# Kernel optimization log

Measured on AMD Instinct MI355X. Metric: run time of the kernel, lower is better.

## Reference

```python
import jax, jax.numpy as jnp
import numpy as np
import math

B = 2
D_MODEL = 2048
L_MAX = 4096
FILTER_ORDER = 64
EMB_DIM = 3
SHORT_K = 3


def setup_inputs() -> dict:
    key = jax.random.key(0)
    ks = jax.random.split(key, 16)
    D = D_MODEL

    def n(k, shape, scale=0.02):
        return jax.random.normal(k, shape, dtype=jnp.float32) * scale

    return {
        "x": jax.random.normal(ks[0], (B, L_MAX, D), dtype=jnp.float32),
        "in_proj_w": n(ks[1], (3 * D, D)),
        "in_proj_b": n(ks[2], (3 * D,)),
        "short_w": n(ks[3], (3 * D, 1, SHORT_K), 0.3),   # depthwise conv weight (O, I/groups=1, K)
        "short_b": n(ks[4], (3 * D,), 0.1),
        "mlp_w0": n(ks[5], (FILTER_ORDER, EMB_DIM), 0.5),
        "mlp_b0": n(ks[6], (FILTER_ORDER,), 0.5),
        "sin_freq": jnp.ones((1, FILTER_ORDER), dtype=jnp.float32),  # Sin module, w=1, shared across MLP layers
        "mlp_w1": n(ks[7], (FILTER_ORDER, FILTER_ORDER), 0.1),
        "mlp_b1": n(ks[8], (FILTER_ORDER,), 0.1),
        "mlp_w2": n(ks[9], (FILTER_ORDER, FILTER_ORDER), 0.1),
        "mlp_b2": n(ks[10], (FILTER_ORDER,), 0.1),
        "mlp_w3": n(ks[11], (D, FILTER_ORDER), 0.1),      # final Linear(order -> d_model, bias=False)
        "filter_bias": jax.random.normal(ks[12], (D,), dtype=jnp.float32),  # HyenaFilter.bias ~ randn
        "out_proj_w": n(ks[13], (D, D)),
        "out_proj_b": n(ks[14], (D,)),
    }


def _pos_emb(L):
    # PositionalEmbedding: t in [0,1], 1 complex band (emb_dim=3 -> bands=1)
    t = jnp.linspace(0.0, 1.0, L)[:, None]               # (L, 1)
    t_resc = jnp.linspace(0.0, L - 1.0, L)
    w = 2.0 * math.pi * t_resc / L                       # (L,)
    bands = (EMB_DIM - 1) // 2
    f = jnp.linspace(1e-4, bands - 1.0, bands)           # (bands,)
    ang = f[None, :] * w[:, None]                        # (L, bands)
    # z = exp(-1j * f * w) -> real = cos, imag = -sin
    z = jnp.concatenate([t, jnp.cos(ang), -jnp.sin(ang)], axis=-1)  # (L, 3)
    return z, t


def _filter_k(L, w0, b0, freq, w1, b1, w2, b2, w3):
    z, t = _pos_emb(L)
    h = jnp.sin(freq * (z @ w0.T + b0))
    h = jnp.sin(freq * (h @ w1.T + b1))
    h = jnp.sin(freq * (h @ w2.T + b2))
    h = h @ w3.T                                         # (L, D)
    # ExponentialModulation: deltas = linspace(log(.01)/1.5, log(.01)/0.3, D)
    max_decay = math.log(0.01) / 0.3
    min_decay = math.log(0.01) / 1.5
    deltas = jnp.linspace(min_decay, max_decay, h.shape[-1])
    decay = jnp.exp(-t * jnp.abs(deltas)[None, :])       # (L, D)
    return (h * decay).T                                 # (D, L)


def _fftconv(u, k, bias):
    # fftconv_ref with gelu=False, no dropout_mask: u (B, D, L), k (D, L), bias (D,)
    L = u.shape[-1]
    n = 2 * L
    k_f = jnp.fft.rfft(k, n=n) / n                       # (D, L+1)
    u_f = jnp.fft.rfft(u, n=n)                           # (B, D, L+1)
    y = jnp.fft.irfft(u_f * k_f, n=n, norm="forward")[..., :L]
    return y + u * bias[:, None]


def reference(x, in_proj_w, in_proj_b, short_w, short_b, mlp_w0, mlp_b0, sin_freq,
              mlp_w1, mlp_b1, mlp_w2, mlp_b2, mlp_w3, filter_bias,
              out_proj_w, out_proj_b):
    Bn, L, D = x.shape
    u = x @ in_proj_w.T + in_proj_b                      # (B, L, 3D)
    u = jnp.transpose(u, (0, 2, 1))                      # (B, 3D, L)
    # depthwise short conv, padding = short_k - 1, truncate to L (causal-ish)
    uc = jax.lax.conv_general_dilated(
        u, short_w, window_strides=(1,),
        padding=[(SHORT_K - 1, SHORT_K - 1)],
        feature_group_count=3 * D,
        dimension_numbers=("NCH", "OIH", "NCH"))
    uc = uc[..., :L] + short_b[None, :, None]
    x0, x1, v = jnp.split(uc, 3, axis=1)                 # each (B, D, L)
    k = _filter_k(L, mlp_w0, mlp_b0, sin_freq, mlp_w1, mlp_b1, mlp_w2, mlp_b2, mlp_w3)
    # order=2 Hyena recurrence: single gated long-conv step
    v = v * x1
    v = _fftconv(v, k, filter_bias)
    y = v * x0                                           # (B, D, L)
    y = jnp.transpose(y, (0, 2, 1))                      # (B, L, D)
    return y @ out_proj_w.T + out_proj_b
```

## Files before the change

### kernel.cpp

```cpp
#include <hip/hip_runtime.h>
#include <hip/hip_bf16.h>
#include <cstdint>
#include <cstddef>

typedef __attribute__((ext_vector_type(8))) short    bf16x8;
typedef __attribute__((ext_vector_type(4))) float    f32x4;
typedef __attribute__((ext_vector_type(8))) unsigned short u16x8;
typedef __attribute__((ext_vector_type(4))) float    f32v4;
typedef __attribute__((ext_vector_type(4))) unsigned short u16v4;

__device__ __forceinline__ float b2f(unsigned short v) {
    return __builtin_bit_cast(float, ((unsigned int)v) << 16);
}
__device__ __forceinline__ unsigned short f2b(float f) {
    unsigned int u = __builtin_bit_cast(unsigned int, f);
    u += 0x7fffu + ((u >> 16) & 1u);
    return (unsigned short)(u >> 16);
}

__device__ __forceinline__ void async16(const void* g, void* l) {
    __builtin_amdgcn_global_load_lds(
        (const __attribute__((address_space(1))) unsigned int*)g,
        (__attribute__((address_space(3))) unsigned int*)l, 16, 0, 0);
}

__global__ __launch_bounds__(256) void cvt_f32_bf16(const float* __restrict__ src,
                                                    unsigned short* __restrict__ dst, int n4) {
    int i = blockIdx.x * blockDim.x + threadIdx.x;
    int stride = gridDim.x * blockDim.x;
    const f32v4* s4 = (const f32v4*)src;
    u16v4* d4 = (u16v4*)dst;
    for (; i < n4; i += stride) {
        f32v4 v = s4[i];
        u16v4 o;
        o.x = f2b(v.x); o.y = f2b(v.y); o.z = f2b(v.z); o.w = f2b(v.w);
        d4[i] = o;
    }
}

template <int MODE>
__global__ __launch_bounds__(512, 1) void gemm256(
    const unsigned short* __restrict__ A,
    const unsigned short* __restrict__ Bw,
    const float* __restrict__ bias,
    void* __restrict__ Cout,
    int M, int N, int K, int Lseq, int CH, int ntn)
{
    constexpr int SMEM_BYTES = (MODE == 1) ? 135168 : 131072;
    __shared__ char smemc[SMEM_BYTES];

    const int tid = threadIdx.x;
    const int w   = tid >> 6;
    const int l   = tid & 63;
    const int wm  = w & 1;
    const int wn  = w >> 1;
    const int quad = l >> 4;
    const int lq   = l & 15;

    int id = blockIdx.x;
    const int q8 = gridDim.x >> 3;
    id = (id & 7) * q8 + (id >> 3);
    const int bx = id % ntn, by = id / ntn;
    const int n0 = bx * 256, m0 = by * 256;

    const int su0 = quad ^ (lq & 7);
    const int su1 = su0 ^ 4;

    uint32_t offAe[2][2], offBe[2][2];
    int dA[2][2], dB[2][2];
    #pragma unroll
    for (int h = 0; h < 2; ++h)
        #pragma unroll
        for (int c = 0; c < 2; ++c) {
            const int Lr = h * 128 + w * 16 + c * 8 + (l >> 3);
            const int gA = ((Lr & 64) << 1) | ((Lr & 128) >> 1) | (Lr & 63);
            const int u  = (l & 7) ^ (l >> 3);
            offAe[h][c] = (uint32_t)(m0 + gA) * (uint32_t)K + (uint32_t)(u * 8);
            offBe[h][c] = (uint32_t)(n0 + Lr) * (uint32_t)K + (uint32_t)(u * 8);
            const int rb = (h * 128 + w * 16 + c * 8) * 128;
            dA[h][c] = rb;
            dB[h][c] = 32768 + rb;
        }

#define STAGE_A(bs, h, tile) do { \
    async16(A + offAe[h][0] + (size_t)(tile) * 64, smemc + ((bs) * 65536 + dA[h][0])); \
    async16(A + offAe[h][1] + (size_t)(tile) * 64, smemc + ((bs) * 65536 + dA[h][1])); \
} while (0)
#define STAGE_B(bs, h, tile) do { \
    async16(Bw + offBe[h][0] + (size_t)(tile) * 64, smemc + ((bs) * 65536 + dB[h][0])); \
    async16(Bw + offBe[h][1] + (size_t)(tile) * 64, smemc + ((bs) * 65536 + dB[h][1])); \
} while (0)

    f32x4 acc[8][4] = {};
    bf16x8 bw[4][2], a[2][2];

#define LDB8(bs) do { \
    _Pragma("unroll") for (int j = 0; j < 4; ++j) { \
        const int Lr = wn * 64 + j * 16 + lq; \
        bw[j][0] = *(const bf16x8*)(smemc + (bs) * 65536 + 32768 + Lr * 128 + su0 * 16); \
        bw[j][1] = *(const bf16x8*)(smemc + (bs) * 65536 + 32768 + Lr * 128 + su1 * 16); \
    } } while (0)
#define LDA4(bs, q) do { \
    _Pragma("unroll") for (int mf = 0; mf < 2; ++mf) { \
        const int g = wm * 128 + (q) * 32 + mf * 16 + lq; \
        const int Lr = ((g & 64) << 1) | ((g & 128) >> 1) | (g & 63); \
        a[mf][0] = *(const bf16x8*)(smemc + (bs) * 65536 + Lr * 128 + su0 * 16); \
        a[mf][1] = *(const bf16x8*)(smemc + (bs) * 65536 + Lr * 128 + su1 * 16); \
    } } while (0)
#define MFMA16(q) do { \
    _Pragma("unroll") for (int mf = 0; mf < 2; ++mf) \
    _Pragma("unroll") for (int j = 0; j < 4; ++j) \
    _Pragma("unroll") for (int kk = 0; kk < 2; ++kk) \
        acc[(q) * 2 + mf][j] = __builtin_amdgcn_mfma_f32_16x16x32_bf16(a[mf][kk], bw[j][kk], acc[(q) * 2 + mf][j], 0, 0, 0); \
} while (0)
#define PHASE_SYNC() do { \
    __builtin_amdgcn_s_barrier(); \
    asm volatile("s_waitcnt lgkmcnt(0)" ::: "memory"); \
    __builtin_amdgcn_sched_barrier(0); \
    __builtin_amdgcn_s_setprio(1); \
} while (0)
#define PHASE_END() do { \
    __builtin_amdgcn_s_setprio(0); \
    __builtin_amdgcn_s_barrier(); \
} while (0)
#define PHASE_END_DRAIN(lastf) do { \
    __builtin_amdgcn_s_setprio(0); \
    if (lastf) asm volatile("s_waitcnt vmcnt(0)" ::: "memory"); \
    else       asm volatile("s_waitcnt vmcnt(6)" ::: "memory"); \
    __builtin_amdgcn_s_barrier(); \
} while (0)

    STAGE_B(0, 0, 0); STAGE_B(0, 1, 0); STAGE_A(0, 0, 0); STAGE_A(0, 1, 0);
    STAGE_B(1, 0, 1); STAGE_B(1, 1, 1); STAGE_A(1, 0, 1);
    asm volatile("s_waitcnt vmcnt(6)" ::: "memory");
    __builtin_amdgcn_s_barrier();

    const int nIt = K >> 7;
    for (int i = 0; i < nIt; ++i) {
        const bool last = (i == nIt - 1);
        const int t0 = 2 * i, t1 = 2 * i + 1;
        LDB8(0); LDA4(0, 0); STAGE_A(1, 1, t1);
        PHASE_SYNC(); MFMA16(0); PHASE_END();
        LDA4(0, 1); if (!last) STAGE_B(0, 0, t0 + 2);
        PHASE_SYNC(); MFMA16(1); PHASE_END();
        LDA4(0, 2); if (!last) STAGE_B(0, 1, t0 + 2);
        PHASE_SYNC(); MFMA16(2); PHASE_END();
        LDA4(0, 3); if (!last) STAGE_A(0, 0, t0 + 2);
        PHASE_SYNC(); MFMA16(3); PHASE_END_DRAIN(last);
        LDB8(1); LDA4(1, 0); if (!last) STAGE_A(0, 1, t0 + 2);
        PHASE_SYNC(); MFMA16(0); PHASE_END();
        LDA4(1, 1); if (!last) STAGE_B(1, 0, t1 + 2);
        PHASE_SYNC(); MFMA16(1); PHASE_END();
        LDA4(1, 2); if (!last) STAGE_B(1, 1, t1 + 2);
        PHASE_SYNC(); MFMA16(2); PHASE_END();
        LDA4(1, 3); if (!last) STAGE_A(1, 0, t1 + 2);
        PHASE_SYNC(); MFMA16(3); PHASE_END_DRAIN(last);
    }

    if (MODE == 0) {
        float* out = (float*)Cout;
        #pragma unroll
        for (int j = 0; j < 4; ++j) {
            const int col = n0 + wn * 64 + j * 16 + lq;
            const float bv = bias[col];
            #pragma unroll
            for (int i8 = 0; i8 < 8; ++i8) {
                const int rowb = m0 + wm * 128 + i8 * 16 + quad * 4;
                f32x4 c = acc[i8][j];
                out[(size_t)(rowb + 0) * N + col] = c.x + bv;
                out[(size_t)(rowb + 1) * N + col] = c.y + bv;
                out[(size_t)(rowb + 2) * N + col] = c.z + bv;
                out[(size_t)(rowb + 3) * N + col] = c.w + bv;
            }
        }
    } else {
        unsigned short* sE = (unsigned short*)smemc;
        __syncthreads();
        #pragma unroll
        for (int j = 0; j < 4; ++j) {
            const int nl = wn * 64 + j * 16 + lq;
            const float bv = bias[n0 + nl];
            #pragma unroll
            for (int i8 = 0; i8 < 8; ++i8) {
                const int ml = wm * 128 + i8 * 16 + quad * 4;
                f32x4 c = acc[i8][j];
                u16v4 pk;
                pk.x = f2b(c.x + bv); pk.y = f2b(c.y + bv);
                pk.z = f2b(c.z + bv); pk.w = f2b(c.w + bv);
                *(u16v4*)&sE[nl * 264 + ml] = pk;
            }
        }
        __syncthreads();
        unsigned short* uo = (unsigned short*)Cout;
        const int bI = m0 >> 12;
        const int l0 = m0 & 4095;
        for (int e = tid; e < 8192; e += 512) {
            const int nl = e >> 5, seg = e & 31;
            u16x8 v = *(const u16x8*)&sE[nl * 264 + seg * 8];
            *(u16x8*)&uo[(size_t)(bI * CH + n0 + nl) * Lseq + l0 + seg * 8] = v;
        }
    }
#undef STAGE_A
#undef STAGE_B
#undef LDB8
#undef LDA4
#undef MFMA16
#undef PHASE_SYNC
#undef PHASE_END
#undef PHASE_END_DRAIN
}

__global__ __launch_bounds__(256) void filter_kernel(
    const float* __restrict__ w0, const float* __restrict__ b0,
    const float* __restrict__ freq,
    const float* __restrict__ w1, const float* __restrict__ b1,
    const float* __restrict__ w2, const float* __restrict__ b2,
    const float* __restrict__ w3, float* __restrict__ kf)
{
    __shared__ float ha[64][64];
    __shared__ float hb[64][64];
    const int tid = threadIdx.x;
    const int l0 = blockIdx.x * 64;
    const int d0 = blockIdx.y * 256;
    const int l  = tid & 63;
    const int lg = l0 + l;
    const float tt = (float)lg * (1.0f / 4095.0f);
    const float wang = 6.283185307179586f * (float)lg * (1.0f / 4096.0f);
    const float a  = 1e-4f * wang;
    const float z0 = tt, z1 = cosf(a), z2 = -sinf(a);

    for (int e = tid; e < 4096; e += 256) {
        const int dim = e >> 6;
        float pre = z0 * w0[dim * 3] + z1 * w0[dim * 3 + 1] + z2 * w0[dim * 3 + 2] + b0[dim];
        ha[dim][l] = sinf(freq[dim] * pre);
    }
    __syncthreads();
    for (int e = tid; e < 4096; e += 256) {
        const int dim = e >> 6;
        float acc = b1[dim];
        #pragma unroll
        for (int jj = 0; jj < 64; ++jj) acc += w1[dim * 64 + jj] * ha[jj][l];
        hb[dim][l] = sinf(freq[dim] * acc);
    }
    __syncthreads();
    for (int e = tid; e < 4096; e += 256) {
        const int dim = e >> 6;
        float acc = b2[dim];
        #pragma unroll
        for (int jj = 0; jj < 64; ++jj) acc += w2[dim * 64 + jj] * hb[jj][l];
        ha[dim][l] = sinf(freq[dim] * acc);
    }
    __syncthreads();
    for (int d = d0 + (tid >> 6); d < d0 + 256; d += 4) {
        float acc = 0.f;
        #pragma unroll
        for (int jj = 0; jj < 64; ++jj) acc += w3[d * 64 + jj] * ha[jj][l];
        const float delta = fabsf(-3.0701134573253944f + (-5.999245642062483e-3f) * (float)d);
        kf[(size_t)d * 4096 + lg] = acc * __expf(-tt * delta);
    }
}

#define PIDX(i) ((i) + ((i) >> 5))

__device__ __forceinline__ void bfly_f(float& r1, float& i1, float& r2, float& i2, float wr, float wi) {
    float ur = r1, ui = i1, vr = r2, vi = i2;
    r1 = ur + vr; i1 = ui + vi;
    float dr = ur - vr, di = ui - vi;
    r2 = dr * wr - di * wi;
    i2 = dr * wi + di * wr;
}
__device__ __forceinline__ void bfly_i(float& r1, float& i1, float& r2, float& i2, float wr, float wi) {
    float vr = r2 * wr - i2 * wi, vi = r2 * wi + i2 * wr;
    float ur = r1, ui = i1;
    r1 = ur + vr; i1 = ui + vi;
    r2 = ur - vr; i2 = ui - vi;
}

template <int DS, int STR>
__device__ __forceinline__ void fwd_stage(float* re, float* im, int tt) {
    float wr[8], wi[8];
    constexpr float c = -3.14159265358979f / (float)(STR * DS);
    #pragma unroll
    for (int k = 0; k < DS; ++k) __sincosf(c * (float)(tt + STR * k), &wi[k], &wr[k]);
    #pragma unroll
    for (int s = 0; s < 16; ++s)
        if ((s & DS) == 0)
            bfly_f(re[s], im[s], re[s + DS], im[s + DS], wr[s & (DS - 1)], wi[s & (DS - 1)]);
}
template <int DS, int STR>
__device__ __forceinline__ void inv_stage(float* re, float* im, int tt) {
    float wr[8], wi[8];
    constexpr float c = 3.14159265358979f / (float)(STR * DS);
    #pragma unroll
    for (int k = 0; k < DS; ++k) __sincosf(c * (float)(tt + STR * k), &wi[k], &wr[k]);
    #pragma unroll
    for (int s = 0; s < 16; ++s)
        if ((s & DS) == 0)
            bfly_i(re[s], im[s], re[s + DS], im[s + DS], wr[s & (DS - 1)], wi[s & (DS - 1)]);
}

__device__ __forceinline__ void xchg(float* re, float* im, float* fre, float* fim,
                                     int wbase, int wstr, int rbase, int rstr) {
    __syncthreads();
    #pragma unroll
    for (int s = 0; s < 16; ++s) {
        const int i = wbase + wstr * s;
        fre[PIDX(i)] = re[s]; fim[PIDX(i)] = im[s];
    }
    __syncthreads();
    #pragma unroll
    for (int s = 0; s < 16; ++s) {
        const int i = rbase + rstr * s;
        re[s] = fre[PIDX(i)]; im[s] = fim[PIDX(i)];
    }
}

__device__ __forceinline__ void fwd_fft(float* re, float* im, float* fre, float* fim, int t) {
    const int off = t & 31, seg = t >> 5;
    fwd_stage<8, 512>(re, im, t);
    fwd_stage<4, 512>(re, im, t);
    fwd_stage<2, 512>(re, im, t);
    fwd_stage<1, 512>(re, im, t);
    xchg(re, im, fre, fim, t, 512, seg * 512 + off, 32);
    fwd_stage<8, 32>(re, im, off);
    fwd_stage<4, 32>(re, im, off);
    fwd_stage<2, 32>(re, im, off);
    fwd_stage<1, 32>(re, im, off);
    {
        float wr, wi;
        __sincosf(-3.14159265358979f * (float)(off & 15) / 16.0f, &wi, &wr);
        const bool hi = (off & 16) != 0;
        #pragma unroll
        for (int s = 0; s < 16; ++s) {
            float rr = __shfl_xor(re[s], 16);
            float ri = __shfl_xor(im[s], 16);
            if (!hi) { re[s] += rr; im[s] += ri; }
            else {
                float dr = rr - re[s], di = ri - im[s];
                re[s] = dr * wr - di * wi;
                im[s] = dr * wi + di * wr;
            }
        }
    }
    xchg(re, im, fre, fim, seg * 512 + off, 32, 16 * t, 1);
    fwd_stage<8, 1>(re, im, 0);
    fwd_stage<4, 1>(re, im, 0);
    fwd_stage<2, 1>(re, im, 0);
    fwd_stage<1, 1>(re, im, 0);
}

__device__ __forceinline__ void inv_fft(float* re, float* im, float* fre, float* fim, int t) {
    const int off = t & 31, seg = t >> 5;
    inv_stage<1, 1>(re, im, 0);
    inv_stage<2, 1>(re, im, 0);
    inv_stage<4, 1>(re, im, 0);
    inv_stage<8, 1>(re, im, 0);
    xchg(re, im, fre, fim, 16 * t, 1, seg * 512 + off, 32);
    {
        float wr, wi;
        __sincosf(3.14159265358979f * (float)(off & 15) / 16.0f, &wi, &wr);
        const bool hi = (off & 16) != 0;
        #pragma unroll
        for (int s = 0; s < 16; ++s) {
            float rr = __shfl_xor(re[s], 16);
            float ri = __shfl_xor(im[s], 16);
            if (!hi) {
                float vr = rr * wr - ri * wi, vi = rr * wi + ri * wr;
                re[s] += vr; im[s] += vi;
            } else {
                float vr = re[s] * wr - im[s] * wi, vi = re[s] * wi + im[s] * wr;
                re[s] = rr - vr; im[s] = ri - vi;
            }
        }
    }
    inv_stage<1, 32>(re, im, off);
    inv_stage<2, 32>(re, im, off);
    inv_stage<4, 32>(re, im, off);
    inv_stage<8, 32>(re, im, off);
    xchg(re, im, fre, fim, seg * 512 + off, 32, t, 512);
    inv_stage<1, 512>(re, im, t);
    inv_stage<2, 512>(re, im, t);
    inv_stage<4, 512>(re, im, t);
    inv_stage<8, 512>(re, im, t);
}

__global__ __launch_bounds__(512, 2) void kfft_kernel(
    const float* __restrict__ kf,
    float* __restrict__ kspec)
{
    __shared__ float fre[8448];
    __shared__ float fim[8448];
    const int t = threadIdx.x;
    const int d = blockIdx.x;
    float kr[16], ki[16];
    #pragma unroll
    for (int s = 0; s < 16; ++s) {
        kr[s] = (s < 8) ? kf[(size_t)d * 4096 + t + 512 * s] : 0.f;
        ki[s] = 0.f;
    }
    fwd_fft(kr, ki, fre, fim, t);
    f32x4* kv = (f32x4*)kspec + (size_t)d * 4096 + t;
    #pragma unroll
    for (int q = 0; q < 8; ++q) {
        f32x4 o;
        o.x = kr[2 * q]; o.y = ki[2 * q];
        o.z = kr[2 * q + 1]; o.w = ki[2 * q + 1];
        kv[q * 512] = o;
    }
}

__global__ __launch_bounds__(512, 2) void hyena_fft_kernel(
    const unsigned short* __restrict__ u,
    const float* __restrict__ kspec,
    const float* __restrict__ sw,
    const float* __restrict__ sbv,
    const float* __restrict__ fbias,
    unsigned short* __restrict__ zb)
{
    __shared__ float fre[8448];
    __shared__ float fim[8448];
    const int t = threadIdx.x;
    const int d = blockIdx.x;

    const int c0 = d, c1 = 2048 + d, c2 = 4096 + d;
    const float w00 = sw[c0*3+0], w01 = sw[c0*3+1], w02 = sw[c0*3+2], bb0 = sbv[c0];
    const float w10 = sw[c1*3+0], w11 = sw[c1*3+1], w12 = sw[c1*3+2], bb1 = sbv[c1];
    const float w20 = sw[c2*3+0], w21 = sw[c2*3+1], w22 = sw[c2*3+2], bb2 = sbv[c2];
    const float fb = fbias[d];

    float vgr_[2][8], x0r_[2][8];
    float xr[16], xi[16];
    #pragma unroll
    for (int s = 0; s < 8; ++s) {
        const int l = t + (s << 9);
        #pragma unroll
        for (int b = 0; b < 2; ++b) {
            const size_t base = (size_t)b * 6144 * 4096;
            const size_t r0 = base + (size_t)c0 * 4096;
            const size_t r1 = base + (size_t)c1 * 4096;
            const size_t r2 = base + (size_t)c2 * 4096;
            const float a0 = b2f(u[r0 + l]);
            const float a1 = (l >= 1) ? b2f(u[r0 + l - 1]) : 0.f;
            const float a2 = (l >= 2) ? b2f(u[r0 + l - 2]) : 0.f;
            const float x0v = w00 * a2 + w01 * a1 + w02 * a0 + bb0;
            const float e0 = b2f(u[r1 + l]);
            const float e1 = (l >= 1) ? b2f(u[r1 + l - 1]) : 0.f;
            const float e2 = (l >= 2) ? b2f(u[r1 + l - 2]) : 0.f;
            const float x1v = w10 * e2 + w11 * e1 + w12 * e0 + bb1;
            const float g0 = b2f(u[r2 + l]);
            const float g1 = (l >= 1) ? b2f(u[r2 + l - 1]) : 0.f;
            const float g2 = (l >= 2) ? b2f(u[r2 + l - 2]) : 0.f;
            const float vv = w20 * g2 + w21 * g1 + w22 * g0 + bb2;
            const float vg = vv * x1v;
            vgr_[b][s] = vg; x0r_[b][s] = x0v;
            if (b == 0) xr[s] = vg; else xi[s] = vg;
        }
    }
    #pragma unroll
    for (int s = 8; s < 16; ++s) { xr[s] = 0.f; xi[s] = 0.f; }

    fwd_fft(xr, xi, fre, fim, t);
    {
        const f32x4* kv = (const f32x4*)kspec + (size_t)d * 4096 + t;
        f32x4 kk[8];
        #pragma unroll
        for (int q = 0; q < 8; ++q) kk[q] = kv[q * 512];
        #pragma unroll
        for (int q = 0; q < 8; ++q) {
            float cr = xr[2 * q], ci = xi[2 * q];
            xr[2 * q] = cr * kk[q].x - ci * kk[q].y;
            xi[2 * q] = cr * kk[q].y + ci * kk[q].x;
            cr = xr[2 * q + 1]; ci = xi[2 * q + 1];
            xr[2 * q + 1] = cr * kk[q].z - ci * kk[q].w;
            xi[2 * q + 1] = cr * kk[q].w + ci * kk[q].z;
        }
    }
    inv_fft(xr, xi, fre, fim, t);

    const float inv_n = 1.0f / 8192.0f;
    #pragma unroll
    for (int s = 0; s < 8; ++s) {
        const int p = t + (s << 9);
        const float z0 = (xr[s] * inv_n + vgr_[0][s] * fb) * x0r_[0][s];
        const float z1 = (xi[s] * inv_n + vgr_[1][s] * fb) * x0r_[1][s];
        zb[(size_t)d * 4096 + p]          = f2b(z0);
        zb[(size_t)(2048 + d) * 4096 + p] = f2b(z1);
    }
}

__global__ __launch_bounds__(256) void transpose_kernel(const unsigned short* __restrict__ zb,
                                                        unsigned short* __restrict__ zt)
{
    __shared__ unsigned int tile[64][65];
    const int l0 = blockIdx.x * 64, d0 = blockIdx.y * 64, b = blockIdx.z;
    const int tid = threadIdx.x;
    for (int e = tid; e < 4096; e += 256) {
        const int r = e >> 6, c = e & 63;
        tile[r][c] = zb[(size_t)(b * 2048 + d0 + r) * 4096 + l0 + c];
    }
    __syncthreads();
    for (int e = tid; e < 4096; e += 256) {
        const int r = e >> 6, c = e & 63;
        zt[(size_t)(b * 4096 + l0 + r) * 2048 + d0 + c] = (unsigned short)tile[c][r];
    }
}

extern "C" void kernel_launch(void* const* d_in, const int* in_sizes, int n_in,
                              void* d_out, int out_size, void* d_ws, size_t ws_size,
                              hipStream_t stream)
{
    const float* x   = (const float*)d_in[0];
    const float* ipw = (const float*)d_in[1];
    const float* ipb = (const float*)d_in[2];
    const float* sw  = (const float*)d_in[3];
    const float* sb  = (const float*)d_in[4];
    const float* w0  = (const float*)d_in[5];
    const float* b0  = (const float*)d_in[6];
    const float* fr  = (const float*)d_in[7];
    const float* w1  = (const float*)d_in[8];
    const float* b1  = (const float*)d_in[9];
    const float* w2  = (const float*)d_in[10];
    const float* b2  = (const float*)d_in[11];
    const float* w3  = (const float*)d_in[12];
    const float* fb  = (const float*)d_in[13];
    const float* opw = (const float*)d_in[14];
    const float* opb = (const float*)d_in[15];
    float* out = (float*)d_out;

    char* ws = (char*)d_ws;
    unsigned short* xb    = (unsigned short*)ws;
    unsigned short* wbi   = (unsigned short*)(ws + 33554432);
    float*          kspec = (float*)ws;
    unsigned short* ztb   = (unsigned short*)ws;
    unsigned short* wbo   = (unsigned short*)(ws + 33554432);
    unsigned short* ub    = (unsigned short*)(ws + 134217728);
    float*          kf    = (float*)(ws + 234881024);
    unsigned short* zbm   = (unsigned short*)(ws + 234881024);

    cvt_f32_bf16<<<1024, 256, 0, stream>>>(x,   xb,  16777216 / 4);
    cvt_f32_bf16<<<1024, 256, 0, stream>>>(ipw, wbi, 12582912 / 4);

    gemm256<1><<<768, 512, 0, stream>>>(xb, wbi, ipb, ub, 8192, 6144, 2048, 4096, 6144, 24);

    filter_kernel<<<dim3(64, 8), 256, 0, stream>>>(w0, b0, fr, w1, b1, w2, b2, w3, kf);

    kfft_kernel<<<2048, 512, 0, stream>>>(kf, kspec);

    hyena_fft_kernel<<<2048, 512, 0, stream>>>(ub, kspec, sw, sb, fb, zbm);

    transpose_kernel<<<dim3(64, 32, 2), 256, 0, stream>>>(zbm, ztb);

    cvt_f32_bf16<<<512,  256, 0, stream>>>(opw, wbo, 4194304 / 4);

    gemm256<0><<<256, 512, 0, stream>>>(ztb, wbo, opb, out, 8192, 2048, 2048, 4096, 2048, 8);
}
```

Before: 765.9 us.

## Vectorize hyena FFT global loads/stores via LDS redistribution and wider padding

Result: faster. 749.9 us (-2.1%).

```diff
diff --git a/kernel.cpp b/kernel.cpp
--- a/kernel.cpp
+++ b/kernel.cpp
@@ -260,7 +260,7 @@
     }
 }
 
-#define PIDX(i) ((i) + ((i) >> 5))
+#define PIDX(i) ((i) + (((i) >> 5) << 2))
 
 __device__ __forceinline__ void bfly_f(float& r1, float& i1, float& r2, float& i2, float wr, float wi) {
     float ur = r1, ui = i1, vr = r2, vi = i2;
@@ -302,16 +302,37 @@
 __device__ __forceinline__ void xchg(float* re, float* im, float* fre, float* fim,
                                      int wbase, int wstr, int rbase, int rstr) {
     __syncthreads();
-    #pragma unroll
-    for (int s = 0; s < 16; ++s) {
-        const int i = wbase + wstr * s;
-        fre[PIDX(i)] = re[s]; fim[PIDX(i)] = im[s];
-    }
-    __syncthreads();
-    #pragma unroll
-    for (int s = 0; s < 16; ++s) {
-        const int i = rbase + rstr * s;
-        re[s] = fre[PIDX(i)]; im[s] = fim[PIDX(i)];
+    if (wstr == 1) {
+        #pragma unroll
+        for (int q = 0; q < 4; ++q) {
+            f32x4 vr, vi;
+            vr.x = re[4*q+0]; vr.y = re[4*q+1]; vr.z = re[4*q+2]; vr.w = re[4*q+3];
+            vi.x = im[4*q+0]; vi.y = im[4*q+1]; vi.z = im[4*q+2]; vi.w = im[4*q+3];
+            *(f32x4*)&fre[PIDX(wbase + 4*q)] = vr;
+            *(f32x4*)&fim[PIDX(wbase + 4*q)] = vi;
+        }
+    } else {
+        #pragma unroll
+        for (int s = 0; s < 16; ++s) {
+            const int i = wbase + wstr * s;
+            fre[PIDX(i)] = re[s]; fim[PIDX(i)] = im[s];
+        }
+    }
+    __syncthreads();
+    if (rstr == 1) {
+        #pragma unroll
+        for (int q = 0; q < 4; ++q) {
+            f32x4 vr = *(const f32x4*)&fre[PIDX(rbase + 4*q)];
+            f32x4 vi = *(const f32x4*)&fim[PIDX(rbase + 4*q)];
+            re[4*q+0] = vr.x; re[4*q+1] = vr.y; re[4*q+2] = vr.z; re[4*q+3] = vr.w;
+            im[4*q+0] = vi.x; im[4*q+1] = vi.y; im[4*q+2] = vi.z; im[4*q+3] = vi.w;
+        }
+    } else {
+        #pragma unroll
+        for (int s = 0; s < 16; ++s) {
+            const int i = rbase + rstr * s;
+            re[s] = fre[PIDX(i)]; im[s] = fim[PIDX(i)];
+        }
     }
 }
 
@@ -388,8 +409,8 @@
     const float* __restrict__ kf,
     float* __restrict__ kspec)
 {
-    __shared__ float fre[8448];
-    __shared__ float fim[8448];
+    __shared__ __align__(16) float fre[9216];
+    __shared__ __align__(16) float fim[9216];
     const int t = threadIdx.x;
     const int d = blockIdx.x;
     float kr[16], ki[16];
@@ -407,6 +428,21 @@
         o.z = kr[2 * q + 1]; o.w = ki[2 * q + 1];
         kv[q * 512] = o;
     }
+}
+
+__device__ __forceinline__ void conv8(const unsigned short* __restrict__ row, int lb,
+                                      float W0, float W1, float W2, float BB,
+                                      float* __restrict__ out) {
+    u16x8 v8 = *(const u16x8*)(row + lb);
+    float f[8];
+    #pragma unroll
+    for (int j = 0; j < 8; ++j) f[j] = b2f(v8[j]);
+    const float fm1 = (lb >= 1) ? b2f(row[lb - 1]) : 0.f;
+    const float fm2 = (lb >= 2) ? b2f(row[lb - 2]) : 0.f;
+    out[0] = W0 * fm2 + W1 * fm1 + W2 * f[0] + BB;
+    out[1] = W0 * fm1 + W1 * f[0] + W2 * f[1] + BB;
+    #pragma unroll
+    for (int j = 2; j < 8; ++j) out[j] = W0 * f[j - 2] + W1 * f[j - 1] + W2 * f[j] + BB;
 }
 
 __global__ __launch_bounds__(512, 2) void hyena_fft_kernel(
@@ -417,10 +453,11 @@
     const float* __restrict__ fbias,
     unsigned short* __restrict__ zb)
 {
-    __shared__ float fre[8448];
-    __shared__ float fim[8448];
+    __shared__ __align__(16) float fre[9216];
+    __shared__ __align__(16) float fim[9216];
     const int t = threadIdx.x;
     const int d = blockIdx.x;
+    const int lb = t << 3;
 
     const int c0 = d, c1 = 2048 + d, c2 = 4096 + d;
     const float w00 = sw[c0*3+0], w01 = sw[c0*3+1], w02 = sw[c0*3+2], bb0 = sbv[c0];
@@ -428,33 +465,32 @@
     const float w20 = sw[c2*3+0], w21 = sw[c2*3+1], w22 = sw[c2*3+2], bb2 = sbv[c2];
     const float fb = fbias[d];
 
-    float vgr_[2][8], x0r_[2][8];
+    float vgc[2][8], x0c[2][8];
+    #pragma unroll
+    for (int b = 0; b < 2; ++b) {
+        const size_t base = (size_t)b * 6144 * 4096;
+        float a_[8], e_[8], g_[8];
+        conv8(u + base + (size_t)c0 * 4096, lb, w00, w01, w02, bb0, a_);
+        conv8(u + base + (size_t)c1 * 4096, lb, w10, w11, w12, bb1, e_);
+        conv8(u + base + (size_t)c2 * 4096, lb, w20, w21, w22, bb2, g_);
+        #pragma unroll
+        for (int j = 0; j < 8; ++j) { x0c[b][j] = a_[j]; vgc[b][j] = g_[j] * e_[j]; }
+    }
+
+    #pragma unroll
+    for (int q = 0; q < 2; ++q) {
+        f32x4 vr, vi;
+        vr.x = vgc[0][4*q+0]; vr.y = vgc[0][4*q+1]; vr.z = vgc[0][4*q+2]; vr.w = vgc[0][4*q+3];
+        vi.x = vgc[1][4*q+0]; vi.y = vgc[1][4*q+1]; vi.z = vgc[1][4*q+2]; vi.w = vgc[1][4*q+3];
+        *(f32x4*)&fre[PIDX(lb + 4*q)] = vr;
+        *(f32x4*)&fim[PIDX(lb + 4*q)] = vi;
+    }
+    __syncthreads();
     float xr[16], xi[16];
     #pragma unroll
     for (int s = 0; s < 8; ++s) {
-        const int l = t + (s << 9);
-        #pragma unroll
-        for (int b = 0; b < 2; ++b) {
-            const size_t base = (size_t)b * 6144 * 4096;
-            const size_t r0 = base + (size_t)c0 * 4096;
-            const size_t r1 = base + (size_t)c1 * 4096;
-            const size_t r2 = base + (size_t)c2 * 4096;
-            const float a0 = b2f(u[r0 + l]);
-            const float a1 = (l >= 1) ? b2f(u[r0 + l - 1]) : 0.f;
-            const float a2 = (l >= 2) ? b2f(u[r0 + l - 2]) : 0.f;
-            const float x0v = w00 * a2 + w01 * a1 + w02 * a0 + bb0;
-            const float e0 = b2f(u[r1 + l]);
-            const float e1 = (l >= 1) ? b2f(u[r1 + l - 1]) : 0.f;
-            const float e2 = (l >= 2) ? b2f(u[r1 + l - 2]) : 0.f;
-            const float x1v = w10 * e2 + w11 * e1 + w12 * e0 + bb1;
-            const float g0 = b2f(u[r2 + l]);
-            const float g1 = (l >= 1) ? b2f(u[r2 + l - 1]) : 0.f;
-            const float g2 = (l >= 2) ? b2f(u[r2 + l - 2]) : 0.f;
-            const float vv = w20 * g2 + w21 * g1 + w22 * g0 + bb2;
-            const float vg = vv * x1v;
-            vgr_[b][s] = vg; x0r_[b][s] = x0v;
-            if (b == 0) xr[s] = vg; else xi[s] = vg;
-        }
+        xr[s] = fre[PIDX(t + (s << 9))];
+        xi[s] = fim[PIDX(t + (s << 9))];
     }
     #pragma unroll
     for (int s = 8; s < 16; ++s) { xr[s] = 0.f; xi[s] = 0.f; }
@@ -477,15 +513,30 @@
     }
     inv_fft(xr, xi, fre, fim, t);
 
+    __syncthreads();
+    #pragma unroll
+    for (int s = 0; s < 8; ++s) {
+        fre[PIDX(t + (s << 9))] = xr[s];
+        fim[PIDX(t + (s << 9))] = xi[s];
+    }
+    __syncthreads();
+    float yr[8], yi[8];
+    #pragma unroll
+    for (int q = 0; q < 2; ++q) {
+        f32x4 vr = *(const f32x4*)&fre[PIDX(lb + 4*q)];
+        f32x4 vi = *(const f32x4*)&fim[PIDX(lb + 4*q)];
+        yr[4*q+0] = vr.x; yr[4*q+1] = vr.y; yr[4*q+2] = vr.z; yr[4*q+3] = vr.w;
+        yi[4*q+0] = vi.x; yi[4*q+1] = vi.y; yi[4*q+2] = vi.z; yi[4*q+3] = vi.w;
+    }
     const float inv_n = 1.0f / 8192.0f;
-    #pragma unroll
-    for (int s = 0; s < 8; ++s) {
-        const int p = t + (s << 9);
-        const float z0 = (xr[s] * inv_n + vgr_[0][s] * fb) * x0r_[0][s];
-        const float z1 = (xi[s] * inv_n + vgr_[1][s] * fb) * x0r_[1][s];
-        zb[(size_t)d * 4096 + p]          = f2b(z0);
-        zb[(size_t)(2048 + d) * 4096 + p] = f2b(z1);
-    }
+    u16x8 z0v, z1v;
+    #pragma unroll
+    for (int j = 0; j < 8; ++j) {
+        z0v[j] = (unsigned short)f2b((yr[j] * inv_n + vgc[0][j] * fb) * x0c[0][j]);
+        z1v[j] = (unsigned short)f2b((yi[j] * inv_n + vgc[1][j] * fb) * x0c[1][j]);
+    }
+    *(u16x8*)&zb[(size_t)d * 4096 + lb]          = z0v;
+    *(u16x8*)&zb[(size_t)(2048 + d) * 4096 + lb] = z1v;
 }
 
 __global__ __launch_bounds__(256) void transpose_kernel(const unsigned short* __restrict__ zb,
```
